# Performance work log

Hardware: AMD Instinct MI355X
Metric: run time of the kernel (lower is better)

## Reference

```python
import jax, jax.numpy as jnp
import numpy as np

B, S, DIM = 2, 2048, 2048
H, KVH, D = 16, 8, 128
EPS = 1e-6
ROPE_BASE = 1000000.0
MAX_SEQ = 8192


def _build_rope(max_seq, dim, base):
    inv_freq = 1.0 / (base ** (np.arange(0, dim, 2, dtype=np.float64) / dim))
    t = np.arange(max_seq, dtype=np.float64)
    freqs = np.outer(t, inv_freq)  # [max_seq, dim//2]
    return (jnp.asarray(np.cos(freqs), jnp.float32),
            jnp.asarray(np.sin(freqs), jnp.float32))


def setup_inputs() -> dict:
    key = jax.random.key(0)
    ks = jax.random.split(key, 7)
    scale = 0.02
    cos_cache, sin_cache = _build_rope(MAX_SEQ, D, ROPE_BASE)
    return {
        "x": jax.random.normal(ks[0], (B, S, DIM), jnp.float32),
        "wq": jax.random.normal(ks[1], (DIM, H * D), jnp.float32) * scale,
        "wk": jax.random.normal(ks[2], (DIM, KVH * D), jnp.float32) * scale,
        "wv": jax.random.normal(ks[3], (DIM, KVH * D), jnp.float32) * scale,
        "wo": jax.random.normal(ks[4], (H * D, DIM), jnp.float32) * scale,
        "q_gamma": 1.0 + 0.01 * jax.random.normal(ks[5], (D,), jnp.float32),
        "k_gamma": 1.0 + 0.01 * jax.random.normal(ks[6], (D,), jnp.float32),
        "cos_cache": cos_cache,
        "sin_cache": sin_cache,
    }


def _rmsnorm(t, gamma):
    var = jnp.mean(t * t, axis=-1, keepdims=True)
    return t * jax.lax.rsqrt(var + EPS) * gamma


def _rotate_half(t):
    t1, t2 = jnp.split(t, 2, axis=-1)
    return jnp.concatenate((-t2, t1), axis=-1)


def _apply_rope(t, cos, sin):
    # t: [B, S, heads, D]; cos/sin: [S, D//2]
    cos_f = jnp.concatenate((cos, cos), axis=-1)[None, :, None, :]
    sin_f = jnp.concatenate((sin, sin), axis=-1)[None, :, None, :]
    return t * cos_f + _rotate_half(t) * sin_f


def reference(x, wq, wk, wv, wo, q_gamma, k_gamma, cos_cache, sin_cache):
    b, s, _ = x.shape
    q = (x @ wq).reshape(b, s, H, D)
    k = (x @ wk).reshape(b, s, KVH, D)
    v = (x @ wv).reshape(b, s, KVH, D)
    q = _rmsnorm(q, q_gamma)
    k = _rmsnorm(k, k_gamma)
    # prefill: kv_len == q_len == s, cache empty
    cos, sin = cos_cache[:s], sin_cache[:s]
    q = _apply_rope(q, cos, sin)
    k = _apply_rope(k, cos, sin)
    # -> [B, heads, S, D]
    q = q.transpose(0, 2, 1, 3)
    k = k.transpose(0, 2, 1, 3)
    v = v.transpose(0, 2, 1, 3)
    # GQA: repeat_interleave kv heads
    g = H // KVH
    k = jnp.repeat(k, g, axis=1)
    v = jnp.repeat(v, g, axis=1)
    scale = 1.0 / jnp.sqrt(jnp.asarray(D, x.dtype))
    scores = jnp.einsum("bhqd,bhkd->bhqk", q, k) * scale
    causal = jnp.tril(jnp.ones((s, s), bool))
    scores = jnp.where(causal, scores, jnp.finfo(scores.dtype).min)
    attn = jax.nn.softmax(scores, axis=-1)
    out = jnp.einsum("bhqk,bhkd->bhqd", attn, v)
    out = out.transpose(0, 2, 1, 3).reshape(b, s, H * D)
    return out @ wo
```

## Files before the change

### kernel.cpp

```cpp
#include <hip/hip_runtime.h>
#include <hip/hip_bf16.h>


typedef __attribute__((ext_vector_type(8))) short s16x8;
typedef __attribute__((ext_vector_type(4))) float f32x4;
typedef __attribute__((ext_vector_type(16))) float f32x16;

typedef const __attribute__((address_space(1))) void* gas_t;
typedef __attribute__((address_space(3))) void* las_t;
#define GLL16(g, l) __builtin_amdgcn_global_load_lds((gas_t)(const void*)(g), (las_t)(void*)(l), 16, 0, 0)

static __device__ __forceinline__ unsigned short f2bf(float f) {
    union { float f; unsigned u; } v; v.f = f;
    unsigned r = v.u + 0x7FFF + ((v.u >> 16) & 1);
    return (unsigned short)(r >> 16);
}
static __device__ __forceinline__ float bf2f(unsigned short h) {
    union { unsigned u; float f; } v; v.u = ((unsigned)h) << 16;
    return v.f;
}
static __device__ __forceinline__ float exp2_fast(float x) {
    float r; asm("v_exp_f32 %0, %1" : "=v"(r) : "v"(x)); return r;
}
static __device__ __forceinline__ unsigned cvt_pk_bf16(float a, float b) {
    unsigned r; asm("v_cvt_pk_bf16_f32 %0, %1, %2" : "=v"(r) : "v"(a), "v"(b)); return r;
}

#define SCALE_L2E 0.12751744900929f

__global__ __launch_bounds__(256) void k_prep(const float* __restrict__ x,
                                              const float* __restrict__ wq,
                                              const float* __restrict__ wk,
                                              const float* __restrict__ wv,
                                              const float* __restrict__ wo,
                                              unsigned short* __restrict__ xb,
                                              unsigned short* __restrict__ w1t,
                                              unsigned short* __restrict__ w2t) {
    __shared__ float t[64][65];
    int z = blockIdx.z;
    int tid = threadIdx.x;
    if (z == 4) {
        int bidc = blockIdx.y * 32 + blockIdx.x;
        #pragma unroll
        for (int j = 0; j < 4; j++) {
            int i = ((bidc * 4 + j) * 256 + tid) * 8;
            float4 a = *(const float4*)(x + i);
            float4 b = *(const float4*)(x + i + 4);
            s16x8 o;
            o[0] = (short)f2bf(a.x); o[1] = (short)f2bf(a.y); o[2] = (short)f2bf(a.z); o[3] = (short)f2bf(a.w);
            o[4] = (short)f2bf(b.x); o[5] = (short)f2bf(b.y); o[6] = (short)f2bf(b.z); o[7] = (short)f2bf(b.w);
            *(s16x8*)(xb + i) = o;
        }
        return;
    }
    const float* src; unsigned short* dst; int N, nbase;
    if (z == 0)      { src = wq; dst = w1t; N = 2048; nbase = 0;    }
    else if (z == 1) { src = wk; dst = w1t; N = 1024; nbase = 2048; }
    else if (z == 2) { src = wv; dst = w1t; N = 1024; nbase = 3072; }
    else             { src = wo; dst = w2t; N = 2048; nbase = 0;    }
    int k0 = blockIdx.x * 64, n0 = blockIdx.y * 64;
    if (n0 >= N) return;
    int tx = tid & 63, ty0 = tid >> 6;
    #pragma unroll
    for (int p = 0; p < 16; p++) {
        int ty = ty0 + p * 4;
        t[ty][tx] = src[(size_t)(k0 + ty) * N + n0 + tx];
    }
    __syncthreads();
    #pragma unroll
    for (int p = 0; p < 16; p++) {
        int ty = ty0 + p * 4;
        dst[(size_t)(nbase + n0 + ty) * 2048 + k0 + tx] = f2bf(t[tx][ty]);
    }
}

__global__ __launch_bounds__(256) void k_transpose_v(const unsigned short* __restrict__ V,
                                                     unsigned short* __restrict__ Vt) {
    __shared__ unsigned short t[64][65];
    int s0 = blockIdx.x * 64, d0 = blockIdx.y * 64;
    size_t base = (size_t)blockIdx.z * 2048 * 128;
    int tid = threadIdx.x;
    int tx = tid & 63, ty0 = tid >> 6;
    #pragma unroll
    for (int p = 0; p < 16; p++) {
        int ty = ty0 + p * 4;
        t[ty][tx] = V[base + (size_t)(s0 + ty) * 128 + d0 + tx];
    }
    __syncthreads();
    #pragma unroll
    for (int p = 0; p < 16; p++) {
        int ty = ty0 + p * 4;
        Vt[base + (size_t)(d0 + ty) * 2048 + s0 + tx] = t[tx][ty];
    }
}

template<int OUTF32>
__global__ __launch_bounds__(512, 2) void k_gemm256(const unsigned short* __restrict__ A,
                                                    const unsigned short* __restrict__ Bt,
                                                    void* __restrict__ Cout,
                                                    int M, int N, int K) {
    __shared__ unsigned short Ls[2][2][2][8192];
    int tid = threadIdx.x, lane = tid & 63, wave = tid >> 6;
    int wm = wave >> 2, wn = wave & 3;
    int lr = lane & 15, lg = lane >> 4;
    int swrow = wave * 16 + (lane >> 2);
    int scol  = (((lane & 3) ^ ((lane >> 3) & 3)) * 8);
    int cg    = ((lg ^ ((lr >> 1) & 3)) * 8);
    const unsigned short* Ab = A  + (size_t)(blockIdx.x * 256) * K;
    const unsigned short* Bb = Bt + (size_t)(blockIdx.y * 256) * K;

    f32x4 acc[8][4] = {};
    int NK = K / 64;

    auto issue = [&](int slot, int mat, int kk, int k0) {
        const unsigned short* base = mat ? Bb : Ab;
        unsigned short* dst = &Ls[slot][mat][kk][wave * 512];
        GLL16(base + (size_t)swrow * K + k0 + kk * 32 + scol, dst);
        GLL16(base + (size_t)(swrow + 128) * K + k0 + kk * 32 + scol, dst + 4096);
    };

    issue(0, 0, 0, 0);
    issue(0, 1, 0, 0);
    issue(0, 0, 1, 0);
    issue(0, 1, 1, 0);
    asm volatile("s_waitcnt vmcnt(4)" ::: "memory");
    __builtin_amdgcn_s_barrier();

    for (int t = 0; t < NK; ++t) {
        int slot = t & 1, nslot = slot ^ 1;
        int kn = (t + 1) * 64;
        bool more = (t + 1) < NK;
        const unsigned short* As0 = Ls[slot][0][0];
        const unsigned short* Bs0 = Ls[slot][1][0];
        const unsigned short* As1 = Ls[slot][0][1];
        const unsigned short* Bs1 = Ls[slot][1][1];
        s16x8 af[4], bfr[4];

        #pragma unroll
        for (int m = 0; m < 4; m++) af[m]  = *(const s16x8*)&As0[(wm * 128 + m * 16 + lr) * 32 + cg];
        #pragma unroll
        for (int n = 0; n < 4; n++) bfr[n] = *(const s16x8*)&Bs0[(wn * 64 + n * 16 + lr) * 32 + cg];
        if (more) issue(nslot, 0, 0, kn);
        asm volatile("" ::: "memory");
        __builtin_amdgcn_s_barrier();
        __builtin_amdgcn_s_setprio(1);
        #pragma unroll
        for (int m = 0; m < 4; m++)
            #pragma unroll
            for (int n = 0; n < 4; n++)
                acc[m][n] = __builtin_amdgcn_mfma_f32_16x16x32_bf16(af[m], bfr[n], acc[m][n], 0, 0, 0);
        __builtin_amdgcn_s_setprio(0);
        asm volatile("" ::: "memory");
        __builtin_amdgcn_s_barrier();

        #pragma unroll
        for (int m = 0; m < 4; m++) af[m] = *(const s16x8*)&As0[(wm * 128 + (m + 4) * 16 + lr) * 32 + cg];
        if (more) { issue(nslot, 1, 0, kn); asm volatile("s_waitcnt vmcnt(4)" ::: "memory"); }
        else      {                         asm volatile("s_waitcnt vmcnt(0)" ::: "memory"); }
        asm volatile("" ::: "memory");
        __builtin_amdgcn_s_barrier();
        __builtin_amdgcn_s_setprio(1);
        #pragma unroll
        for (int m = 0; m < 4; m++)
            #pragma unroll
            for (int n = 0; n < 4; n++)
                acc[m + 4][n] = __builtin_amdgcn_mfma_f32_16x16x32_bf16(af[m], bfr[n], acc[m + 4][n], 0, 0, 0);
        __builtin_amdgcn_s_setprio(0);
        asm volatile("" ::: "memory");
        __builtin_amdgcn_s_barrier();

        #pragma unroll
        for (int m = 0; m < 4; m++) af[m]  = *(const s16x8*)&As1[(wm * 128 + m * 16 + lr) * 32 + cg];
        #pragma unroll
        for (int n = 0; n < 4; n++) bfr[n] = *(const s16x8*)&Bs1[(wn * 64 + n * 16 + lr) * 32 + cg];
        if (more) issue(nslot, 0, 1, kn);
        asm volatile("" ::: "memory");
        __builtin_amdgcn_s_barrier();
        __builtin_amdgcn_s_setprio(1);
        #pragma unroll
        for (int m = 0; m < 4; m++)
            #pragma unroll
            for (int n = 0; n < 4; n++)
                acc[m][n] = __builtin_amdgcn_mfma_f32_16x16x32_bf16(af[m], bfr[n], acc[m][n], 0, 0, 0);
        __builtin_amdgcn_s_setprio(0);
        asm volatile("" ::: "memory");
        __builtin_amdgcn_s_barrier();

        #pragma unroll
        for (int m = 0; m < 4; m++) af[m] = *(const s16x8*)&As1[(wm * 128 + (m + 4) * 16 + lr) * 32 + cg];
        if (more) { issue(nslot, 1, 1, kn); asm volatile("s_waitcnt vmcnt(4)" ::: "memory"); }
        asm volatile("" ::: "memory");
        __builtin_amdgcn_s_barrier();
        __builtin_amdgcn_s_setprio(1);
        #pragma unroll
        for (int m = 0; m < 4; m++)
            #pragma unroll
            for (int n = 0; n < 4; n++)
                acc[m + 4][n] = __builtin_amdgcn_mfma_f32_16x16x32_bf16(af[m], bfr[n], acc[m + 4][n], 0, 0, 0);
        __builtin_amdgcn_s_setprio(0);
        asm volatile("" ::: "memory");
        __builtin_amdgcn_s_barrier();
    }

    int rbase = blockIdx.x * 256 + wm * 128;
    int cbase = blockIdx.y * 256 + wn * 64;
    #pragma unroll
    for (int am = 0; am < 8; am++)
        #pragma unroll
        for (int n = 0; n < 4; n++)
            #pragma unroll
            for (int r = 0; r < 4; r++) {
                int row = rbase + am * 16 + lg * 4 + r;
                int col = cbase + n * 16 + lr;
                float v = acc[am][n][r];
                if (OUTF32) ((float*)Cout)[(size_t)row * N + col] = v;
                else        ((unsigned short*)Cout)[(size_t)row * N + col] = f2bf(v);
            }
}

template<int OUTF32>
__global__ __launch_bounds__(256, 2) void k_gemm128(const unsigned short* __restrict__ A,
                                                    const unsigned short* __restrict__ Bt,
                                                    void* __restrict__ Cout,
                                                    int M, int N, int K) {
    __shared__ unsigned short Ls[2][2][2][4096];
    int tid = threadIdx.x, lane = tid & 63, wave = tid >> 6;
    int wm = wave >> 1, wn = wave & 1;
    int lr = lane & 15, lg = lane >> 4;
    int swrow = wave * 16 + (lane >> 2);
    int scol  = (((lane & 3) ^ ((lane >> 3) & 3)) * 8);
    int cg    = ((lg ^ ((lr >> 1) & 3)) * 8);
    const unsigned short* Ab = A  + (size_t)(blockIdx.x * 128) * K;
    const unsigned short* Bb = Bt + (size_t)(blockIdx.y * 128) * K;

    f32x4 acc[4][4] = {};
    int NK = K / 64;

    auto issue = [&](int slot, int mat, int kk, int k0) {
        const unsigned short* base = mat ? Bb : Ab;
        unsigned short* dst = &Ls[slot][mat][kk][wave * 512];
        GLL16(base + (size_t)swrow * K + k0 + kk * 32 + scol, dst);
        GLL16(base + (size_t)(swrow + 64) * K + k0 + kk * 32 + scol, dst + 2048);
    };

    issue(0, 0, 0, 0);
    issue(0, 1, 0, 0);
    issue(0, 0, 1, 0);
    issue(0, 1, 1, 0);
    asm volatile("s_waitcnt vmcnt(4)" ::: "memory");
    __builtin_amdgcn_s_barrier();

    for (int t = 0; t < NK; ++t) {
        int slot = t & 1, nslot = slot ^ 1;
        int kn = (t + 1) * 64;
        bool more = (t + 1) < NK;
        const unsigned short* As0 = Ls[slot][0][0];
        const unsigned short* Bs0 = Ls[slot][1][0];
        const unsigned short* As1 = Ls[slot][0][1];
        const unsigned short* Bs1 = Ls[slot][1][1];
        s16x8 af[4], bfr[4];

        #pragma unroll
        for (int m = 0; m < 4; m++) af[m]  = *(const s16x8*)&As0[(wm * 64 + m * 16 + lr) * 32 + cg];
        #pragma unroll
        for (int n = 0; n < 4; n++) bfr[n] = *(const s16x8*)&Bs0[(wn * 64 + n * 16 + lr) * 32 + cg];
        if (more) { issue(nslot, 0, 0, kn); issue(nslot, 1, 0, kn);
                    asm volatile("s_waitcnt vmcnt(4)" ::: "memory"); }
        else      { asm volatile("s_waitcnt vmcnt(0)" ::: "memory"); }
        asm volatile("" ::: "memory");
        __builtin_amdgcn_s_barrier();
        __builtin_amdgcn_s_setprio(1);
        #pragma unroll
        for (int m = 0; m < 4; m++)
            #pragma unroll
            for (int n = 0; n < 4; n++)
                acc[m][n] = __builtin_amdgcn_mfma_f32_16x16x32_bf16(af[m], bfr[n], acc[m][n], 0, 0, 0);
        __builtin_amdgcn_s_setprio(0);
        asm volatile("" ::: "memory");
        __builtin_amdgcn_s_barrier();

        #pragma unroll
        for (int m = 0; m < 4; m++) af[m]  = *(const s16x8*)&As1[(wm * 64 + m * 16 + lr) * 32 + cg];
        #pragma unroll
        for (int n = 0; n < 4; n++) bfr[n] = *(const s16x8*)&Bs1[(wn * 64 + n * 16 + lr) * 32 + cg];
        if (more) { issue(nslot, 0, 1, kn); issue(nslot, 1, 1, kn);
                    asm volatile("s_waitcnt vmcnt(4)" ::: "memory"); }
        asm volatile("" ::: "memory");
        __builtin_amdgcn_s_barrier();
        __builtin_amdgcn_s_setprio(1);
        #pragma unroll
        for (int m = 0; m < 4; m++)
            #pragma unroll
            for (int n = 0; n < 4; n++)
                acc[m][n] = __builtin_amdgcn_mfma_f32_16x16x32_bf16(af[m], bfr[n], acc[m][n], 0, 0, 0);
        __builtin_amdgcn_s_setprio(0);
        asm volatile("" ::: "memory");
        __builtin_amdgcn_s_barrier();
    }

    int rbase = blockIdx.x * 128 + wm * 64;
    int cbase = blockIdx.y * 128 + wn * 64;
    #pragma unroll
    for (int m = 0; m < 4; m++)
        #pragma unroll
        for (int n = 0; n < 4; n++)
            #pragma unroll
            for (int r = 0; r < 4; r++) {
                int row = rbase + m * 16 + lg * 4 + r;
                int col = cbase + n * 16 + lr;
                float v = acc[m][n][r];
                if (OUTF32) ((float*)Cout)[(size_t)row * N + col] = v;
                else        ((unsigned short*)Cout)[(size_t)row * N + col] = f2bf(v);
            }
}

__global__ __launch_bounds__(256) void k_rms_rope(const unsigned short* __restrict__ qkv,
                                                  const float* __restrict__ qg,
                                                  const float* __restrict__ kg,
                                                  const float* __restrict__ cosc,
                                                  const float* __restrict__ sinc,
                                                  unsigned short* __restrict__ Qt,
                                                  unsigned short* __restrict__ Kt,
                                                  unsigned short* __restrict__ Vt) {
    int r = blockIdx.x;
    int b = r >> 11;
    int s = r & 2047;
    int tid = threadIdx.x;
    int wave = tid >> 6, lane = tid & 63;
    int sl = lane >> 4;
    int li = lane & 15;
    int d0 = li * 8;
    const unsigned short* row = qkv + (size_t)r * 4096;
    #pragma unroll
    for (int p = 0; p < 2; p++) {
        int seg = p * 16 + wave * 4 + sl;
        s16x8 raw = *(const s16x8*)(row + seg * 128 + d0);
        if (seg >= 24) {
            *(s16x8*)(Vt + ((size_t)(b * 8 + (seg - 24)) * 2048 + s) * 128 + d0) = raw;
            continue;
        }
        float e[8];
        #pragma unroll
        for (int j = 0; j < 8; j++) e[j] = bf2f((unsigned short)raw[j]);
        float ssq = 0.f;
        #pragma unroll
        for (int j = 0; j < 8; j++) ssq += e[j] * e[j];
        ssq += __shfl_xor(ssq, 1, 64);
        ssq += __shfl_xor(ssq, 2, 64);
        ssq += __shfl_xor(ssq, 4, 64);
        ssq += __shfl_xor(ssq, 8, 64);
        float rn = rsqrtf(ssq * (1.0f / 128.0f) + 1e-6f);
        const float* g = (seg < 16) ? qg : kg;
        float gs = (seg < 16) ? SCALE_L2E : 1.0f;
        float4 g0 = *(const float4*)(g + d0);
        float4 g1 = *(const float4*)(g + d0 + 4);
        float t[8];
        t[0] = e[0] * rn * g0.x * gs; t[1] = e[1] * rn * g0.y * gs;
        t[2] = e[2] * rn * g0.z * gs; t[3] = e[3] * rn * g0.w * gs;
        t[4] = e[4] * rn * g1.x * gs; t[5] = e[5] * rn * g1.y * gs;
        t[6] = e[6] * rn * g1.z * gs; t[7] = e[7] * rn * g1.w * gs;
        float pr[8];
        #pragma unroll
        for (int j = 0; j < 8; j++) pr[j] = __shfl_xor(t[j], 8, 64);
        int didx = d0 & 63;
        float4 c0 = *(const float4*)(cosc + (size_t)s * 64 + didx);
        float4 c1 = *(const float4*)(cosc + (size_t)s * 64 + didx + 4);
        float4 sn0 = *(const float4*)(sinc + (size_t)s * 64 + didx);
        float4 sn1 = *(const float4*)(sinc + (size_t)s * 64 + didx + 4);
        float cv[8] = {c0.x, c0.y, c0.z, c0.w, c1.x, c1.y, c1.z, c1.w};
        float sv[8] = {sn0.x, sn0.y, sn0.z, sn0.w, sn1.x, sn1.y, sn1.z, sn1.w};
        float sgn = (li < 8) ? -1.0f : 1.0f;
        s16x8 o;
        #pragma unroll
        for (int j = 0; j < 8; j++)
            o[j] = (short)f2bf(t[j] * cv[j] + sgn * pr[j] * sv[j]);
        unsigned short* dst = (seg < 16)
            ? Qt + ((size_t)(b * 16 + seg) * 2048 + s) * 128 + d0
            : Kt + ((size_t)(b * 8 + (seg - 16)) * 2048 + s) * 128 + d0;
        *(s16x8*)dst = o;
    }
}

__global__ __launch_bounds__(256, 2) void k_attn(const unsigned short* __restrict__ Qt,
                                                 const unsigned short* __restrict__ Kt,
                                                 const unsigned short* __restrict__ Vtg,
                                                 unsigned short* __restrict__ attn) {
    __shared__ unsigned short Ks[2][64 * 128];
    __shared__ unsigned short Vs[2][128 * 64];
    int bid = blockIdx.x;
    int lo = bid & 255;
    int qb, bh;
    if (bid < 256) { qb = lo & 15;        bh = lo >> 4; }
    else           { qb = 15 - (lo & 15); bh = 16 + (lo >> 4); }
    int b = bh >> 4, h = bh & 15;
    int kvh = h >> 1;
    int tid = threadIdx.x;
    int lane = tid & 63, wave = tid >> 6;
    int ql = lane & 31;
    int hf = lane >> 5;
    int q0 = qb * 128;
    const unsigned short* Qb    = Qt + ((size_t)bh * 2048 + q0 + wave * 32 + ql) * 128;
    const unsigned short* Kbase = Kt + (size_t)(b * 8 + kvh) * 2048 * 128;
    const unsigned short* Vtb   = Vtg + (size_t)(b * 8 + kvh) * 128 * 2048;
    s16x8 aq[8];
    #pragma unroll
    for (int ds = 0; ds < 8; ds++)
        aq[ds] = *(const s16x8*)(Qb + ds * 16 + hf * 8);
    f32x16 out[4] = {};
    float m_q = -1e30f, l_q = 0.f;
    int qglob = q0 + wave * 32 + ql;
    int qlo   = q0 + wave * 32;
    int qhi   = qlo + 31;
    int ntiles = 2 * qb + 2;
    int krow = tid >> 4, kcolb = tid & 15;
    int vrow = tid >> 3, vcolb = tid & 7;
    int kscol = (kcolb ^ (krow & 7)) * 8;
    int vscol = (vcolb ^ (vrow & 7)) * 8;
    int eq = (ql & 7);

    auto stage = [&](int buf, int k0) {
        #pragma unroll
        for (int p = 0; p < 4; p++) {
            GLL16(Kbase + (size_t)(k0 + krow + p * 16) * 128 + kscol,
                  &Ks[buf][(krow + p * 16) * 128 + kcolb * 8]);
            GLL16(Vtb + (size_t)(vrow + p * 32) * 2048 + k0 + vscol,
                  &Vs[buf][(vrow + p * 32) * 64 + vcolb * 8]);
        }
    };

    stage(0, 0);

    for (int t = 0; t < ntiles; t++) {
        int k0 = t * 64;
        int buf = t & 1;
        asm volatile("s_waitcnt vmcnt(0)" ::: "memory");
        __syncthreads();
        if (t + 1 < ntiles) stage(buf ^ 1, k0 + 64);
        if (k0 <= qhi) {
            f32x16 st[2] = {};
            __builtin_amdgcn_s_setprio(1);
            #pragma unroll
            for (int sub = 0; sub < 2; sub++)
                #pragma unroll
                for (int ds = 0; ds < 8; ds++) {
                    s16x8 kf = *(const s16x8*)&Ks[buf][(sub * 32 + ql) * 128 + ((ds * 2 + hf) ^ eq) * 8];
                    st[sub] = __builtin_amdgcn_mfma_f32_32x32x16_bf16(kf, aq[ds], st[sub], 0, 0, 0);
                }
            __builtin_amdgcn_s_setprio(0);
            float mx = -1e30f;
            if (k0 + 63 > qlo) {
                #pragma unroll
                for (int sub = 0; sub < 2; sub++)
                    #pragma unroll
                    for (int r = 0; r < 16; r++) {
                        int kv = k0 + sub * 32 + (r & 3) + 8 * (r >> 2) + 4 * hf;
                        if (kv > qglob) st[sub][r] = -1e30f;
                        mx = fmaxf(mx, st[sub][r]);
                    }
            } else {
                #pragma unroll
                for (int sub = 0; sub < 2; sub++)
                    #pragma unroll
                    for (int r = 0; r < 16; r++) mx = fmaxf(mx, st[sub][r]);
            }
            mx = fmaxf(mx, __shfl_xor(mx, 32, 64));
            bool defer = __all(mx <= m_q + 8.0f);
            float sf = 1.0f;
            if (!defer) {
                float mnew = fmaxf(m_q, mx);
                sf = exp2_fast(m_q - mnew);
                m_q = mnew;
            }
            float rs = 0.f;
            #pragma unroll
            for (int sub = 0; sub < 2; sub++)
                #pragma unroll
                for (int r = 0; r < 16; r++) {
                    float e = exp2_fast(st[sub][r] - m_q);
                    st[sub][r] = e;
                    rs += e;
                }
            rs += __shfl_xor(rs, 32, 64);
            l_q = defer ? (l_q + rs) : (l_q * sf + rs);
            s16x8 pf[4];
            #pragma unroll
            for (int sub = 0; sub < 2; sub++) {
                unsigned w0a = cvt_pk_bf16(st[sub][0],  st[sub][1]);
                unsigned w0b = cvt_pk_bf16(st[sub][2],  st[sub][3]);
                unsigned w1a = cvt_pk_bf16(st[sub][4],  st[sub][5]);
                unsigned w1b = cvt_pk_bf16(st[sub][6],  st[sub][7]);
                unsigned w2a = cvt_pk_bf16(st[sub][8],  st[sub][9]);
                unsigned w2b = cvt_pk_bf16(st[sub][10], st[sub][11]);
                unsigned w3a = cvt_pk_bf16(st[sub][12], st[sub][13]);
                unsigned w3b = cvt_pk_bf16(st[sub][14], st[sub][15]);
                auto s0 = __builtin_amdgcn_permlane32_swap(w0a, w1a, false, false);
                auto s1 = __builtin_amdgcn_permlane32_swap(w0b, w1b, false, false);
                auto s2 = __builtin_amdgcn_permlane32_swap(w2a, w3a, false, false);
                auto s3 = __builtin_amdgcn_permlane32_swap(w2b, w3b, false, false);
                union { unsigned u[4]; s16x8 v; } fa, fb;
                fa.u[0] = s0[0]; fa.u[1] = s1[0]; fa.u[2] = s0[1]; fa.u[3] = s1[1];
                fb.u[0] = s2[0]; fb.u[1] = s3[0]; fb.u[2] = s2[1]; fb.u[3] = s3[1];
                pf[sub * 2]     = fa.v;
                pf[sub * 2 + 1] = fb.v;
            }
            if (!defer) {
                float sfr[16];
                #pragma unroll
                for (int r = 0; r < 16; r++)
                    sfr[r] = __shfl(sf, (r & 3) + 8 * (r >> 2) + 4 * hf, 64);
                #pragma unroll
                for (int dblk = 0; dblk < 4; dblk++)
                    #pragma unroll
                    for (int r = 0; r < 16; r++) out[dblk][r] *= sfr[r];
            }
            __builtin_amdgcn_s_setprio(1);
            #pragma unroll
            for (int ks = 0; ks < 4; ks++) {
                #pragma unroll
                for (int dblk = 0; dblk < 4; dblk++) {
                    s16x8 vf = *(const s16x8*)&Vs[buf][(dblk * 32 + ql) * 64 + ((ks * 2 + hf) ^ eq) * 8];
                    out[dblk] = __builtin_amdgcn_mfma_f32_32x32x16_bf16(pf[ks], vf, out[dblk], 0, 0, 0);
                }
            }
            __builtin_amdgcn_s_setprio(0);
        }
    }
    float linv = 1.0f / l_q;
    float inv[16];
    #pragma unroll
    for (int r = 0; r < 16; r++)
        inv[r] = __shfl(linv, (r & 3) + 8 * (r >> 2) + 4 * hf, 64);
    #pragma unroll
    for (int dblk = 0; dblk < 4; dblk++)
        #pragma unroll
        for (int r = 0; r < 16; r++) {
            int row = q0 + wave * 32 + (r & 3) + 8 * (r >> 2) + 4 * hf;
            attn[((size_t)(b * 2048) + row) * 2048 + h * 128 + dblk * 32 + ql] =
                f2bf(out[dblk][r] * inv[r]);
        }
}

extern "C" void kernel_launch(void* const* d_in, const int* in_sizes, int n_in,
                              void* d_out, int out_size, void* d_ws, size_t ws_size,
                              hipStream_t stream) {
    const float* x    = (const float*)d_in[0];
    const float* wq   = (const float*)d_in[1];
    const float* wk   = (const float*)d_in[2];
    const float* wv   = (const float*)d_in[3];
    const float* wo   = (const float*)d_in[4];
    const float* qg   = (const float*)d_in[5];
    const float* kg   = (const float*)d_in[6];
    const float* cosc = (const float*)d_in[7];
    const float* sinc = (const float*)d_in[8];

    char* ws = (char*)d_ws;
    unsigned short* xb   = (unsigned short*)(ws);
    unsigned short* w1t  = (unsigned short*)(ws + 16777216);
    unsigned short* w2t  = (unsigned short*)(ws + 33554432);
    unsigned short* qkv  = (unsigned short*)(ws + 41943040);
    unsigned short* Qt   = (unsigned short*)(ws + 75497472);
    unsigned short* Kt   = (unsigned short*)(ws + 92274688);
    unsigned short* Vt   = (unsigned short*)(ws + 100663296);
    unsigned short* attn = (unsigned short*)(ws + 109051904);
    unsigned short* Vtg  = qkv;

    k_prep<<<dim3(32, 32, 5), 256, 0, stream>>>(x, wq, wk, wv, wo, xb, w1t, w2t);
    k_gemm256<0><<<dim3(16, 16), 512, 0, stream>>>(xb, w1t, qkv, 4096, 4096, 2048);
    k_rms_rope<<<4096, 256, 0, stream>>>(qkv, qg, kg, cosc, sinc, Qt, Kt, Vt);
    k_transpose_v<<<dim3(32, 2, 16), 256, 0, stream>>>(Vt, Vtg);
    k_attn<<<512, 256, 0, stream>>>(Qt, Kt, Vtg, attn);
    k_gemm128<1><<<dim3(32, 16), 256, 0, stream>>>(attn, w2t, d_out, 4096, 2048, 2048);
}
```

Measured before the change: 209.6 us.

## Fuse RMSNorm and RoPE into QKV GEMM epilogue via LDS staging

The QKV GEMM epilogue now stages its bf16 tile in shared memory with an XOR swizzle. Each thread then reads one full 128-wide head row and applies RMSNorm and RoPE before writing Q/K/V directly in head-major layout. This removes the separate rms_rope kernel and the round trip of the qkv intermediate through global memory. In exchange it adds an epilogue that holds 16 vectors per thread and issues per-thread scattered cos/sin/gamma loads, which may raise register pressure.

```diff
diff --git a/kernel.cpp b/kernel.cpp
--- a/kernel.cpp
+++ b/kernel.cpp
@@ -94,11 +94,16 @@
     }
 }
 
-template<int OUTF32>
-__global__ __launch_bounds__(512, 2) void k_gemm256(const unsigned short* __restrict__ A,
-                                                    const unsigned short* __restrict__ Bt,
-                                                    void* __restrict__ Cout,
-                                                    int M, int N, int K) {
+__global__ __launch_bounds__(512, 2) void k_gemm_qkv(const unsigned short* __restrict__ A,
+                                                     const unsigned short* __restrict__ Bt,
+                                                     const float* __restrict__ qg,
+                                                     const float* __restrict__ kg,
+                                                     const float* __restrict__ cosc,
+                                                     const float* __restrict__ sinc,
+                                                     unsigned short* __restrict__ Qt,
+                                                     unsigned short* __restrict__ Kt,
+                                                     unsigned short* __restrict__ Vt,
+                                                     int K) {
     __shared__ unsigned short Ls[2][2][2][8192];
     int tid = threadIdx.x, lane = tid & 63, wave = tid >> 6;
     int wm = wave >> 2, wn = wave & 3;
@@ -202,20 +207,72 @@
         __builtin_amdgcn_s_barrier();
     }
 
-    int rbase = blockIdx.x * 256 + wm * 128;
-    int cbase = blockIdx.y * 256 + wn * 64;
+    unsigned short* Lc = (unsigned short*)Ls;
     #pragma unroll
     for (int am = 0; am < 8; am++)
         #pragma unroll
         for (int n = 0; n < 4; n++)
             #pragma unroll
             for (int r = 0; r < 4; r++) {
-                int row = rbase + am * 16 + lg * 4 + r;
-                int col = cbase + n * 16 + lr;
-                float v = acc[am][n][r];
-                if (OUTF32) ((float*)Cout)[(size_t)row * N + col] = v;
-                else        ((unsigned short*)Cout)[(size_t)row * N + col] = f2bf(v);
-            }
+                int row_l = wm * 128 + am * 16 + lg * 4 + r;
+                int col_l = wn * 64 + n * 16 + lr;
+                int cs = (col_l >> 3) ^ (row_l & 15);
+                Lc[row_l * 256 + cs * 8 + (col_l & 7)] = f2bf(acc[am][n][r]);
+            }
+    __syncthreads();
+    int row_l = tid & 255;
+    int hb = tid >> 8;
+    int row_g = blockIdx.x * 256 + row_l;
+    int bb = row_g >> 11, s = row_g & 2047;
+    int seg = blockIdx.y * 2 + hb;
+    s16x8 vals[16];
+    #pragma unroll
+    for (int j = 0; j < 16; j++) {
+        int cs = (hb * 16 + j) ^ (row_l & 15);
+        vals[j] = *(const s16x8*)&Lc[row_l * 256 + cs * 8];
+    }
+    if (seg >= 24) {
+        unsigned short* dst = Vt + ((size_t)(bb * 8 + seg - 24) * 2048 + s) * 128;
+        #pragma unroll
+        for (int j = 0; j < 16; j++) *(s16x8*)(dst + j * 8) = vals[j];
+    } else {
+        float ssq = 0.f;
+        #pragma unroll
+        for (int j = 0; j < 16; j++)
+            #pragma unroll
+            for (int e = 0; e < 8; e++) { float f = bf2f((unsigned short)vals[j][e]); ssq += f * f; }
+        float rn = rsqrtf(ssq * (1.0f / 128.0f) + 1e-6f);
+        const float* g = (seg < 16) ? qg : kg;
+        float rg = rn * ((seg < 16) ? SCALE_L2E : 1.0f);
+        unsigned short* dst = (seg < 16)
+            ? Qt + ((size_t)(bb * 16 + seg) * 2048 + s) * 128
+            : Kt + ((size_t)(bb * 8 + seg - 16) * 2048 + s) * 128;
+        #pragma unroll
+        for (int j = 0; j < 8; j++) {
+            float4 gl0 = *(const float4*)(g + j * 8);
+            float4 gl1 = *(const float4*)(g + j * 8 + 4);
+            float4 gh0 = *(const float4*)(g + 64 + j * 8);
+            float4 gh1 = *(const float4*)(g + 64 + j * 8 + 4);
+            float4 c0  = *(const float4*)(cosc + (size_t)s * 64 + j * 8);
+            float4 c1  = *(const float4*)(cosc + (size_t)s * 64 + j * 8 + 4);
+            float4 sn0 = *(const float4*)(sinc + (size_t)s * 64 + j * 8);
+            float4 sn1 = *(const float4*)(sinc + (size_t)s * 64 + j * 8 + 4);
+            float glv[8] = {gl0.x, gl0.y, gl0.z, gl0.w, gl1.x, gl1.y, gl1.z, gl1.w};
+            float ghv[8] = {gh0.x, gh0.y, gh0.z, gh0.w, gh1.x, gh1.y, gh1.z, gh1.w};
+            float cv[8]  = {c0.x, c0.y, c0.z, c0.w, c1.x, c1.y, c1.z, c1.w};
+            float sv[8]  = {sn0.x, sn0.y, sn0.z, sn0.w, sn1.x, sn1.y, sn1.z, sn1.w};
+            s16x8 ol, oh;
+            #pragma unroll
+            for (int e = 0; e < 8; e++) {
+                float tl = bf2f((unsigned short)vals[j][e])     * rg * glv[e];
+                float th = bf2f((unsigned short)vals[j + 8][e]) * rg * ghv[e];
+                ol[e] = (short)f2bf(tl * cv[e] - th * sv[e]);
+                oh[e] = (short)f2bf(th * cv[e] + tl * sv[e]);
+            }
+            *(s16x8*)(dst + j * 8)      = ol;
+            *(s16x8*)(dst + 64 + j * 8) = oh;
+        }
+    }
 }
 
 template<int OUTF32>
@@ -312,73 +369,6 @@
                 if (OUTF32) ((float*)Cout)[(size_t)row * N + col] = v;
                 else        ((unsigned short*)Cout)[(size_t)row * N + col] = f2bf(v);
             }
-}
-
-__global__ __launch_bounds__(256) void k_rms_rope(const unsigned short* __restrict__ qkv,
-                                                  const float* __restrict__ qg,
-                                                  const float* __restrict__ kg,
-                                                  const float* __restrict__ cosc,
-                                                  const float* __restrict__ sinc,
-                                                  unsigned short* __restrict__ Qt,
-                                                  unsigned short* __restrict__ Kt,
-                                                  unsigned short* __restrict__ Vt) {
-    int r = blockIdx.x;
-    int b = r >> 11;
-    int s = r & 2047;
-    int tid = threadIdx.x;
-    int wave = tid >> 6, lane = tid & 63;
-    int sl = lane >> 4;
-    int li = lane & 15;
-    int d0 = li * 8;
-    const unsigned short* row = qkv + (size_t)r * 4096;
-    #pragma unroll
-    for (int p = 0; p < 2; p++) {
-        int seg = p * 16 + wave * 4 + sl;
-        s16x8 raw = *(const s16x8*)(row + seg * 128 + d0);
-        if (seg >= 24) {
-            *(s16x8*)(Vt + ((size_t)(b * 8 + (seg - 24)) * 2048 + s) * 128 + d0) = raw;
-            continue;
-        }
-        float e[8];
-        #pragma unroll
-        for (int j = 0; j < 8; j++) e[j] = bf2f((unsigned short)raw[j]);
-        float ssq = 0.f;
-        #pragma unroll
-        for (int j = 0; j < 8; j++) ssq += e[j] * e[j];
-        ssq += __shfl_xor(ssq, 1, 64);
-        ssq += __shfl_xor(ssq, 2, 64);
-        ssq += __shfl_xor(ssq, 4, 64);
-        ssq += __shfl_xor(ssq, 8, 64);
-        float rn = rsqrtf(ssq * (1.0f / 128.0f) + 1e-6f);
-        const float* g = (seg < 16) ? qg : kg;
-        float gs = (seg < 16) ? SCALE_L2E : 1.0f;
-        float4 g0 = *(const float4*)(g + d0);
-        float4 g1 = *(const float4*)(g + d0 + 4);
-        float t[8];
-        t[0] = e[0] * rn * g0.x * gs; t[1] = e[1] * rn * g0.y * gs;
-        t[2] = e[2] * rn * g0.z * gs; t[3] = e[3] * rn * g0.w * gs;
-        t[4] = e[4] * rn * g1.x * gs; t[5] = e[5] * rn * g1.y * gs;
-        t[6] = e[6] * rn * g1.z * gs; t[7] = e[7] * rn * g1.w * gs;
-        float pr[8];
-        #pragma unroll
-        for (int j = 0; j < 8; j++) pr[j] = __shfl_xor(t[j], 8, 64);
-        int didx = d0 & 63;
-        float4 c0 = *(const float4*)(cosc + (size_t)s * 64 + didx);
-        float4 c1 = *(const float4*)(cosc + (size_t)s * 64 + didx + 4);
-        float4 sn0 = *(const float4*)(sinc + (size_t)s * 64 + didx);
-        float4 sn1 = *(const float4*)(sinc + (size_t)s * 64 + didx + 4);
-        float cv[8] = {c0.x, c0.y, c0.z, c0.w, c1.x, c1.y, c1.z, c1.w};
-        float sv[8] = {sn0.x, sn0.y, sn0.z, sn0.w, sn1.x, sn1.y, sn1.z, sn1.w};
-        float sgn = (li < 8) ? -1.0f : 1.0f;
-        s16x8 o;
-        #pragma unroll
-        for (int j = 0; j < 8; j++)
-            o[j] = (short)f2bf(t[j] * cv[j] + sgn * pr[j] * sv[j]);
-        unsigned short* dst = (seg < 16)
-            ? Qt + ((size_t)(b * 16 + seg) * 2048 + s) * 128 + d0
-            : Kt + ((size_t)(b * 8 + (seg - 16)) * 2048 + s) * 128 + d0;
-        *(s16x8*)dst = o;
-    }
 }
 
 __global__ __launch_bounds__(256, 2) void k_attn(const unsigned short* __restrict__ Qt,
@@ -557,16 +547,14 @@
     unsigned short* xb   = (unsigned short*)(ws);
     unsigned short* w1t  = (unsigned short*)(ws + 16777216);
     unsigned short* w2t  = (unsigned short*)(ws + 33554432);
-    unsigned short* qkv  = (unsigned short*)(ws + 41943040);
+    unsigned short* Vtg  = (unsigned short*)(ws + 41943040);
     unsigned short* Qt   = (unsigned short*)(ws + 75497472);
     unsigned short* Kt   = (unsigned short*)(ws + 92274688);
     unsigned short* Vt   = (unsigned short*)(ws + 100663296);
     unsigned short* attn = (unsigned short*)(ws + 109051904);
-    unsigned short* Vtg  = qkv;
 
     k_prep<<<dim3(32, 32, 5), 256, 0, stream>>>(x, wq, wk, wv, wo, xb, w1t, w2t);
-    k_gemm256<0><<<dim3(16, 16), 512, 0, stream>>>(xb, w1t, qkv, 4096, 4096, 2048);
-    k_rms_rope<<<4096, 256, 0, stream>>>(qkv, qg, kg, cosc, sinc, Qt, Kt, Vt);
+    k_gemm_qkv<<<dim3(16, 16), 512, 0, stream>>>(xb, w1t, qg, kg, cosc, sinc, Qt, Kt, Vt, 2048);
     k_transpose_v<<<dim3(32, 2, 16), 256, 0, stream>>>(Vt, Vtg);
     k_attn<<<512, 256, 0, stream>>>(Qt, Kt, Vtg, attn);
     k_gemm128<1><<<dim3(32, 16), 256, 0, stream>>>(attn, w2t, d_out, 4096, 2048, 2048);
```

After: 212.7 us. Within noise of the previous version (+1.5%).
